# Performance work log

Measured on AMD Instinct MI355X. Metric: run time of the kernel, lower is better.

## Reference

```python
import jax, jax.numpy as jnp
import numpy as np

V, L, H, E, S = 50257, 12, 12, 768, 1024
B, T = 4, 1024
D = E // H
EPS = 1e-5


def setup_inputs() -> dict:
    key = jax.random.key(0)
    ks = jax.random.split(key, 16)
    n = lambda k, shape: (jax.random.normal(k, shape, dtype=jnp.float32) * 0.02)
    return {
        'idx': jax.random.randint(ks[0], (B, T), 0, V),
        'wte': n(ks[1], (V, E)),
        'wpe': n(ks[2], (S, E)),
        'ln1_g': jnp.ones((L, E)), 'ln1_b': jnp.zeros((L, E)),
        'attn_w': n(ks[3], (L, E, 3 * E)), 'attn_b': jnp.zeros((L, 3 * E)),
        'proj_w': n(ks[4], (L, E, E)), 'proj_b': jnp.zeros((L, E)),
        'ln2_g': jnp.ones((L, E)), 'ln2_b': jnp.zeros((L, E)),
        'fc_w': n(ks[5], (L, E, 4 * E)), 'fc_b': jnp.zeros((L, 4 * E)),
        'mproj_w': n(ks[6], (L, 4 * E, E)), 'mproj_b': jnp.zeros((L, E)),
        'lnf_g': jnp.ones((E,)), 'lnf_b': jnp.zeros((E,)),
    }


def layer_norm(x, g, b):
    m = jnp.mean(x, axis=-1, keepdims=True)
    v = jnp.var(x, axis=-1, keepdims=True)
    return (x - m) * jax.lax.rsqrt(v + EPS) * g + b


def reference(idx, wte, wpe, ln1_g, ln1_b, attn_w, attn_b, proj_w, proj_b,
              ln2_g, ln2_b, fc_w, fc_b, mproj_w, mproj_b, lnf_g, lnf_b):
    b, t = idx.shape
    x = wte[idx] + wpe[:t]  # [B,T,E]
    causal = jnp.tril(jnp.ones((t, t), dtype=bool))
    neg_inf = jnp.finfo(x.dtype).min
    for l in range(L):
        h = layer_norm(x, ln1_g[l], ln1_b[l])
        qkv = h @ attn_w[l] + attn_b[l]  # [B,T,3E]
        q, k, v = jnp.split(qkv, 3, axis=-1)
        q = q.reshape(b, t, H, D).transpose(0, 2, 1, 3)  # [B,H,T,D]
        k = k.reshape(b, t, H, D).transpose(0, 2, 1, 3)
        v = v.reshape(b, t, H, D).transpose(0, 2, 1, 3)
        att = jnp.einsum('bhqd,bhkd->bhqk', q, k) / jnp.sqrt(jnp.float32(D))
        att = jnp.where(causal, att, neg_inf)
        att = jax.nn.softmax(att, axis=-1)
        y = jnp.einsum('bhqk,bhkd->bhqd', att, v)
        y = y.transpose(0, 2, 1, 3).reshape(b, t, E)
        x = x + y @ proj_w[l] + proj_b[l]
        h2 = layer_norm(x, ln2_g[l], ln2_b[l])
        h2 = jax.nn.gelu(h2 @ fc_w[l] + fc_b[l], approximate=True)
        x = x + h2 @ mproj_w[l] + mproj_b[l]
    x = layer_norm(x, lnf_g, lnf_b)
    logits = x @ wte.T  # tied lm_head
    return logits
```

## Files before the change

kernel.cpp:

```cpp
#include <hip/hip_runtime.h>
#include <hip/hip_bf16.h>
#include <math.h>

#define VSZ 50257
#define VPAD2 50432
#define NLAYER 12
#define NH 12
#define EMB 768
#define TSEQ 1024
#define NB 4
#define MROWS (NB * TSEQ)
#define DHEAD 64
#define LN_EPS 1e-5f

typedef __attribute__((ext_vector_type(8))) short bf16x8;
typedef __attribute__((ext_vector_type(4))) float f32x4;

__device__ __forceinline__ void load_lds16(const void* g, void* l) {
    __builtin_amdgcn_global_load_lds((const __attribute__((address_space(1))) unsigned int*)g,
                                     (__attribute__((address_space(3))) unsigned int*)l,
                                     16, 0, 0);
}

__global__ void embed_kernel(const int* __restrict__ idx, const float* __restrict__ wte,
                             const float* __restrict__ wpe, float* __restrict__ x) {
    int row = blockIdx.x;
    int t = row & (TSEQ - 1);
    int tok = idx[row];
    const float* wt = wte + (size_t)tok * EMB;
    const float* wp = wpe + (size_t)t * EMB;
    float* xo = x + (size_t)row * EMB;
    for (int e = threadIdx.x; e < EMB; e += blockDim.x)
        xo[e] = wt[e] + wp[e];
}

__global__ void ln_kernel(const float* __restrict__ x, const float* __restrict__ g,
                          const float* __restrict__ b, __hip_bfloat16* __restrict__ out) {
    int row = blockIdx.x;
    const float* xr = x + (size_t)row * EMB;
    __hip_bfloat16* yr = out + (size_t)row * EMB;
    int tid = threadIdx.x;
    float v0 = xr[tid], v1 = xr[tid + 256], v2 = xr[tid + 512];
    float s = v0 + v1 + v2;
    float ss = v0 * v0 + v1 * v1 + v2 * v2;
    #pragma unroll
    for (int i = 1; i < 64; i <<= 1) {
        s  += __shfl_xor(s, i, 64);
        ss += __shfl_xor(ss, i, 64);
    }
    __shared__ float sm[4], sv[4];
    int lane = tid & 63, wid = tid >> 6;
    if (lane == 0) { sm[wid] = s; sv[wid] = ss; }
    __syncthreads();
    float sum = sm[0] + sm[1] + sm[2] + sm[3];
    float sqs = sv[0] + sv[1] + sv[2] + sv[3];
    float mean = sum * (1.0f / EMB);
    float var = sqs * (1.0f / EMB) - mean * mean;
    float rstd = rsqrtf(var + LN_EPS);
    yr[tid]       = __float2bfloat16((v0 - mean) * rstd * g[tid]       + b[tid]);
    yr[tid + 256] = __float2bfloat16((v1 - mean) * rstd * g[tid + 256] + b[tid + 256]);
    yr[tid + 512] = __float2bfloat16((v2 - mean) * rstd * g[tid + 512] + b[tid + 512]);
}

__global__ void ln_acc_kernel(float* __restrict__ x, const float* __restrict__ p0,
                              const float* __restrict__ p1,
                              const float* __restrict__ g, const float* __restrict__ b,
                              __hip_bfloat16* __restrict__ out) {
    int row = blockIdx.x;
    float* xr = x + (size_t)row * EMB;
    const float* q0 = p0 + (size_t)row * EMB;
    const float* q1 = p1 + (size_t)row * EMB;
    __hip_bfloat16* yr = out + (size_t)row * EMB;
    int tid = threadIdx.x;
    float v0 = xr[tid]       + q0[tid]       + q1[tid];
    float v1 = xr[tid + 256] + q0[tid + 256] + q1[tid + 256];
    float v2 = xr[tid + 512] + q0[tid + 512] + q1[tid + 512];
    xr[tid] = v0; xr[tid + 256] = v1; xr[tid + 512] = v2;
    float s = v0 + v1 + v2;
    float ss = v0 * v0 + v1 * v1 + v2 * v2;
    #pragma unroll
    for (int i = 1; i < 64; i <<= 1) {
        s  += __shfl_xor(s, i, 64);
        ss += __shfl_xor(ss, i, 64);
    }
    __shared__ float sm[4], sv[4];
    int lane = tid & 63, wid = tid >> 6;
    if (lane == 0) { sm[wid] = s; sv[wid] = ss; }
    __syncthreads();
    float sum = sm[0] + sm[1] + sm[2] + sm[3];
    float sqs = sv[0] + sv[1] + sv[2] + sv[3];
    float mean = sum * (1.0f / EMB);
    float var = sqs * (1.0f / EMB) - mean * mean;
    float rstd = rsqrtf(var + LN_EPS);
    yr[tid]       = __float2bfloat16((v0 - mean) * rstd * g[tid]       + b[tid]);
    yr[tid + 256] = __float2bfloat16((v1 - mean) * rstd * g[tid + 256] + b[tid + 256]);
    yr[tid + 512] = __float2bfloat16((v2 - mean) * rstd * g[tid + 512] + b[tid + 512]);
}

__global__ void convT4_kernel(const float* __restrict__ aw, const float* __restrict__ pw,
                              const float* __restrict__ fw, const float* __restrict__ mw,
                              __hip_bfloat16* __restrict__ awT, __hip_bfloat16* __restrict__ pwT,
                              __hip_bfloat16* __restrict__ fwT, __hip_bfloat16* __restrict__ mwT) {
    __shared__ float tile[32][33];
    int bid = blockIdx.x;
    const float* W; __hip_bfloat16* Wt; int K, N, t;
    if (bid < 1728)      { W = aw; Wt = awT; K = 768;  N = 2304; t = bid; }
    else if (bid < 2304) { W = pw; Wt = pwT; K = 768;  N = 768;  t = bid - 1728; }
    else if (bid < 4608) { W = fw; Wt = fwT; K = 768;  N = 3072; t = bid - 2304; }
    else                 { W = mw; Wt = mwT; K = 3072; N = 768;  t = bid - 4608; }
    int NT = N >> 5;
    int n0 = (t % NT) << 5, k0 = (t / NT) << 5;
    int tx = threadIdx.x & 31, ty = threadIdx.x >> 5;
    #pragma unroll
    for (int i = ty; i < 32; i += 8)
        tile[i][tx] = W[(size_t)(k0 + i) * N + n0 + tx];
    __syncthreads();
    #pragma unroll
    for (int i = ty; i < 32; i += 8)
        Wt[(size_t)(n0 + i) * K + k0 + tx] = __float2bfloat16(tile[tx][i]);
}

__global__ void conv_wte_kernel(const float* __restrict__ wte, __hip_bfloat16* __restrict__ o) {
    int row = blockIdx.x;
    bool pad = row >= VSZ;
    const float* src = wte + (size_t)row * EMB;
    __hip_bfloat16* dst = o + (size_t)row * EMB;
    for (int e = threadIdx.x; e < EMB; e += blockDim.x)
        dst[e] = __float2bfloat16(pad ? 0.0f : src[e]);
}

template <bool GELU, bool RES, int OUT, bool SPLITK>
__global__ __launch_bounds__(512) void gemm_bt(
                        const __hip_bfloat16* __restrict__ A, const __hip_bfloat16* __restrict__ B,
                        const float* __restrict__ bias, const float* __restrict__ res,
                        float* __restrict__ Cf, __hip_bfloat16* __restrict__ Cb,
                        __hip_bfloat16* __restrict__ vt, float* __restrict__ Cp1,
                        int Kc, int lda, int ldc, int Nclip) {
    __shared__ __hip_bfloat16 Ash[128 * 64];
    __shared__ __hip_bfloat16 Bsh[128 * 64];
    const int tid = threadIdx.x;
    const int lane = tid & 63, wid = tid >> 6;
    const int wr = wid >> 2, wc = wid & 3;

    const int nwg_all = gridDim.x;
    const int cpx = nwg_all >> 3;
    int wg = (blockIdx.x & 7) * cpx + (blockIdx.x >> 3);
    int chunk = 0, nwg = nwg_all;
    if (SPLITK) { chunk = wg & 1; wg >>= 1; nwg = nwg_all >> 1; }
    const int NT = nwg >> 5;
    const int bandsz = NT << 3;
    const int band = wg / bandsz;
    const int rem = wg - band * bandsz;
    const int m0 = (band * 8 + (rem & 7)) * 128;
    const int n0 = (rem >> 3) * 128;
    const int koff = SPLITK ? chunk * Kc : 0;

    f32x4 acc[4][2] = {};
    const int srow = lane >> 3;
    const int scol = ((lane & 7) ^ srow) * 8;

    const int lr16 = lane & 15;
    const int hi = lane >> 4;

    for (int k0 = 0; k0 < Kc; k0 += 64) {
        #pragma unroll
        for (int it = 0; it < 2; ++it) {
            int c = wid + it * 8;
            const __hip_bfloat16* ga = A + (size_t)(m0 + c * 8 + srow) * lda + koff + k0 + scol;
            load_lds16(ga, &Ash[c * 512]);
            const __hip_bfloat16* gb = B + (size_t)(n0 + c * 8 + srow) * lda + koff + k0 + scol;
            load_lds16(gb, &Bsh[c * 512]);
        }
        __syncthreads();
        bf16x8 a[4][2], b[2][2];
        #pragma unroll
        for (int m = 0; m < 4; ++m)
            #pragma unroll
            for (int kk = 0; kk < 2; ++kk) {
                int ra = wr * 64 + m * 16 + lr16;
                int ca = (kk * 32 + hi * 8) ^ ((ra & 7) * 8);
                a[m][kk] = *(const bf16x8*)&Ash[ra * 64 + ca];
            }
        #pragma unroll
        for (int n = 0; n < 2; ++n)
            #pragma unroll
            for (int kk = 0; kk < 2; ++kk) {
                int rb = wc * 32 + n * 16 + lr16;
                int cb = (kk * 32 + hi * 8) ^ ((rb & 7) * 8);
                b[n][kk] = *(const bf16x8*)&Bsh[rb * 64 + cb];
            }
        #pragma unroll
        for (int kk = 0; kk < 2; ++kk)
            #pragma unroll
            for (int m = 0; m < 4; ++m)
                #pragma unroll
                for (int n = 0; n < 2; ++n)
                    acc[m][n] = __builtin_amdgcn_mfma_f32_16x16x32_bf16(a[m][kk], b[n][kk], acc[m][n], 0, 0, 0);
        __syncthreads();
    }

    float* Co = (SPLITK && chunk) ? Cp1 : Cf;
    const bool dobias = bias && (!SPLITK || chunk == 0);
    const int crow0 = m0 + wr * 64, ccol0 = n0 + wc * 32;
    #pragma unroll
    for (int m = 0; m < 4; ++m) {
        #pragma unroll
        for (int n = 0; n < 2; ++n) {
            int col = ccol0 + n * 16 + lr16;
            if (col >= Nclip) continue;
            float bv = dobias ? bias[col] : 0.0f;
            #pragma unroll
            for (int j = 0; j < 4; ++j) {
                int r = crow0 + m * 16 + hi * 4 + j;
                float v = acc[m][n][j] + bv;
                if (GELU) {
                    float t = 0.7978845608028654f * (v + 0.044715f * v * v * v);
                    v = 0.5f * v * (1.0f + tanhf(t));
                }
                if (RES) v += res[(size_t)r * ldc + col];
                if (OUT == 0) Co[(size_t)r * ldc + col] = v;
                else if (OUT == 1) Cb[(size_t)r * ldc + col] = __float2bfloat16(v);
                else {
                    if (col < 2 * EMB) Cb[(size_t)r * (2 * EMB) + col] = __float2bfloat16(v);
                    else {
                        int hh = (col - 2 * EMB) >> 6, dd = (col - 2 * EMB) & 63;
                        int bb = r >> 10, tt = r & 1023;
                        vt[(((size_t)bb * NH + hh) * 64 + dd) * TSEQ + tt] = __float2bfloat16(v);
                    }
                }
            }
        }
    }
}

#define G256_STAGE_A(KT, MH, P) do { \
    int ktw_ = (KT) % 12; \
    load_lds16(A + (size_t)(m0 + (MH) * 64 + srow) * 768 + ktw_ * 64 + sgr8, \
               &lds[(P) * 2][(MH) * 8192 + wid * 512]); \
    load_lds16(A + (size_t)(m0 + 128 + (MH) * 64 + srow) * 768 + ktw_ * 64 + sgr8, \
               &lds[(P) * 2][(MH) * 8192 + 4096 + wid * 512]); \
} while (0)

#define G256_STAGE_B(KT, NH, P) do { \
    int ktw_ = (KT) % 12; \
    load_lds16(Bm + (size_t)(bwc0 * 64 + (NH) * 32 + brow) * 768 + ktw_ * 64 + sgr8, \
               &lds[(P) * 2 + 1][(NH) * 8192 + wid * 512]); \
    load_lds16(Bm + (size_t)((2 + bwc0) * 64 + (NH) * 32 + brow) * 768 + ktw_ * 64 + sgr8, \
               &lds[(P) * 2 + 1][(NH) * 8192 + 4096 + wid * 512]); \
} while (0)

#define G256_PHASE(MH, NH, P, STAGE_STMT, VM) do { \
    bf16x8 af[4][2], bf[2][2]; \
    _Pragma("unroll") \
    for (int f = 0; f < 4; ++f) \
        _Pragma("unroll") \
        for (int kk = 0; kk < 2; ++kk) { \
            int pr = (MH) * 128 + wr * 64 + f * 16 + lr16; \
            af[f][kk] = *(const bf16x8*)((const char*)lds[(P) * 2] + pr * 128 + ((kk * 64 + hi * 16) ^ ((lr16 & 7) << 4))); \
        } \
    _Pragma("unroll") \
    for (int nn = 0; nn < 2; ++nn) \
        _Pragma("unroll") \
        for (int kk = 0; kk < 2; ++kk) { \
            int pr = (NH) * 128 + wc * 32 + nn * 16 + lr16; \
            bf[nn][kk] = *(const bf16x8*)((const char*)lds[(P) * 2 + 1] + pr * 128 + ((kk * 64 + hi * 16) ^ ((lr16 & 7) << 4))); \
        } \
    STAGE_STMT; \
    asm volatile("s_waitcnt vmcnt(" #VM ")" ::: "memory"); \
    __builtin_amdgcn_s_barrier(); \
    asm volatile("s_waitcnt lgkmcnt(0)" ::: "memory"); \
    __builtin_amdgcn_sched_barrier(0); \
    __builtin_amdgcn_s_setprio(1); \
    _Pragma("unroll") \
    for (int kk = 0; kk < 2; ++kk) \
        _Pragma("unroll") \
        for (int f = 0; f < 4; ++f) \
            _Pragma("unroll") \
            for (int nn = 0; nn < 2; ++nn) \
                acc[(MH) * 4 + f][(NH) * 2 + nn] = __builtin_amdgcn_mfma_f32_16x16x32_bf16( \
                    af[f][kk], bf[nn][kk], acc[(MH) * 4 + f][(NH) * 2 + nn], 0, 0, 0); \
    __builtin_amdgcn_s_setprio(0); \
    __builtin_amdgcn_s_barrier(); \
} while (0)

__global__ __launch_bounds__(512, 1) void gemm256(const __hip_bfloat16* __restrict__ A,
                                                  const __hip_bfloat16* __restrict__ Bw,
                                                  float* __restrict__ C) {
    __shared__ __hip_bfloat16 lds[4][16384];
    const int tid = threadIdx.x;
    const int lane = tid & 63, wid = tid >> 6;
    const int wr = wid >> 2, wc = wid & 3;
    const int lr16 = lane & 15, hi = lane >> 4;

    const int bid = blockIdx.x;
    const int wg = (bid & 7) * 394 + (bid >> 3);
    const int band = wg / 1576, rem = wg % 1576;
    const int mt = band * 8 + (rem & 7), nt = rem >> 3;
    const size_t m0 = (size_t)mt * 256;
    const __hip_bfloat16* Bm = Bw + (size_t)nt * 256 * 768;

    const int srow = tid >> 3;
    const int sgr8 = ((tid & 7) ^ ((tid >> 3) & 7)) * 8;
    const int brow = (tid >> 3) & 31;
    const int bwc0 = tid >> 8;

    f32x4 acc[8][4] = {};

    G256_STAGE_A(0, 0, 0);
    G256_STAGE_B(0, 0, 0);
    G256_STAGE_A(0, 1, 0);
    G256_STAGE_B(0, 1, 0);
    G256_STAGE_A(1, 0, 1);
    G256_STAGE_B(1, 0, 1);
    asm volatile("s_waitcnt vmcnt(8)" ::: "memory");
    __builtin_amdgcn_s_barrier();

    for (int kt2 = 0; kt2 < 12; kt2 += 2) {
        G256_PHASE(0, 0, 0, G256_STAGE_A(kt2 + 1, 1, 1), 6);
        G256_PHASE(0, 1, 0, G256_STAGE_B(kt2 + 1, 1, 1), 10);
        G256_PHASE(1, 0, 0, G256_STAGE_A(kt2 + 2, 0, 0), 10);
        G256_PHASE(1, 1, 0, G256_STAGE_B(kt2 + 2, 0, 0), 8);
        G256_PHASE(0, 0, 1, G256_STAGE_A(kt2 + 2, 1, 0), 6);
        G256_PHASE(0, 1, 1, G256_STAGE_B(kt2 + 2, 1, 0), 10);
        G256_PHASE(1, 0, 1, G256_STAGE_A(kt2 + 3, 0, 1), 10);
        G256_PHASE(1, 1, 1, G256_STAGE_B(kt2 + 3, 0, 1), 8);
    }

    const int ccol0 = nt * 256 + wc * 64;
    #pragma unroll
    for (int mf = 0; mf < 8; ++mf) {
        size_t row = m0 + wr * 128 + (mf >> 2) * 64 + (mf & 3) * 16 + hi * 4;
        #pragma unroll
        for (int nf = 0; nf < 4; ++nf) {
            int col = ccol0 + nf * 16 + lr16;
            if (col < VSZ) {
                #pragma unroll
                for (int j = 0; j < 4; ++j)
                    C[(row + j) * VSZ + col] = acc[mf][nf][j];
            }
        }
    }
}

__global__ __launch_bounds__(256) void flash_attn(const __hip_bfloat16* __restrict__ qk,
                                                  const __hip_bfloat16* __restrict__ vT,
                                                  __hip_bfloat16* __restrict__ y) {
    const int qt = blockIdx.x, h = blockIdx.y, b = blockIdx.z;
    const int tid = threadIdx.x;
    const int lane = tid & 63, w = tid >> 6;
    const int g = lane >> 4, lr = lane & 15;

    __shared__ char KshB[64 * 128];
    __shared__ char VshB[64 * 128];
    __shared__ char PshB[4][16 * 128];

    const __hip_bfloat16* qrow = qk + ((size_t)(b * TSEQ + qt * 64 + w * 16 + lr)) * 1536 + h * 64;
    bf16x8 qf0 = *(const bf16x8*)(qrow + g * 8);
    bf16x8 qf1 = *(const bf16x8*)(qrow + 32 + g * 8);

    float m[4], l[4];
    f32x4 o[4];
    #pragma unroll
    for (int j = 0; j < 4; ++j) { m[j] = -1e30f; l[j] = 0.0f; }
    #pragma unroll
    for (int n = 0; n < 4; ++n) o[n] = (f32x4){0.f, 0.f, 0.f, 0.f};

    const int r0 = tid >> 3;
    const int c0 = (tid & 7) * 8;

    for (int kt = 0; kt <= qt; ++kt) {
        __syncthreads();
        #pragma unroll
        for (int it = 0; it < 2; ++it) {
            int r = r0 + it * 32;
            bf16x8 kv = *(const bf16x8*)(qk + ((size_t)(b * TSEQ + kt * 64 + r)) * 1536 + EMB + h * 64 + c0);
            *(bf16x8*)(KshB + ((r * 128 + c0 * 2) ^ ((r & 7) << 4))) = kv;
            bf16x8 vv = *(const bf16x8*)(vT + (((size_t)(b * NH + h)) * 64 + r) * TSEQ + kt * 64 + c0);
            *(bf16x8*)(VshB + ((r * 128 + c0 * 2) ^ ((r & 7) << 4))) = vv;
        }
        __syncthreads();

        f32x4 s[4] = {};
        #pragma unroll
        for (int n = 0; n < 4; ++n) {
            int kr = n * 16 + lr;
            bf16x8 kb0 = *(const bf16x8*)(KshB + ((kr * 128 + g * 16) ^ ((kr & 7) << 4)));
            bf16x8 kb1 = *(const bf16x8*)(KshB + ((kr * 128 + 64 + g * 16) ^ ((kr & 7) << 4)));
            s[n] = __builtin_amdgcn_mfma_f32_16x16x32_bf16(qf0, kb0, s[n], 0, 0, 0);
            s[n] = __builtin_amdgcn_mfma_f32_16x16x32_bf16(qf1, kb1, s[n], 0, 0, 0);
        }

        const bool diag = (kt == qt);
        float tmax[4] = {-1e30f, -1e30f, -1e30f, -1e30f};
        #pragma unroll
        for (int n = 0; n < 4; ++n)
            #pragma unroll
            for (int j = 0; j < 4; ++j) {
                float v = s[n][j] * 0.125f;
                if (diag && (n * 16 + lr > w * 16 + g * 4 + j)) v = -1e30f;
                s[n][j] = v;
                tmax[j] = fmaxf(tmax[j], v);
            }
        #pragma unroll
        for (int j = 0; j < 4; ++j)
            #pragma unroll
            for (int i = 1; i < 16; i <<= 1)
                tmax[j] = fmaxf(tmax[j], __shfl_xor(tmax[j], i, 64));

        float lsum[4] = {0.f, 0.f, 0.f, 0.f};
        float pexp[4][4];
        #pragma unroll
        for (int j = 0; j < 4; ++j) {
            float mn = fmaxf(m[j], tmax[j]);
            float sc = __expf(m[j] - mn);
            l[j] *= sc;
            m[j] = mn;
            #pragma unroll
            for (int n = 0; n < 4; ++n) {
                float p = __expf(s[n][j] - mn);
                pexp[n][j] = p;
                lsum[j] += p;
                o[n][j] *= sc;
            }
        }
        #pragma unroll
        for (int j = 0; j < 4; ++j) {
            #pragma unroll
            for (int i = 1; i < 16; i <<= 1) lsum[j] += __shfl_xor(lsum[j], i, 64);
            l[j] += lsum[j];
        }

        char* P = PshB[w];
        #pragma unroll
        for (int n = 0; n < 4; ++n)
            #pragma unroll
            for (int j = 0; j < 4; ++j) {
                int rw = g * 4 + j;
                *(__hip_bfloat16*)(P + ((rw * 128 + (n * 16 + lr) * 2) ^ ((rw & 7) << 4))) =
                    __float2bfloat16(pexp[n][j]);
            }
        asm volatile("s_waitcnt lgkmcnt(0)" ::: "memory");
        bf16x8 pa0 = *(const bf16x8*)(P + ((lr * 128 + g * 16) ^ ((lr & 7) << 4)));
        bf16x8 pa1 = *(const bf16x8*)(P + ((lr * 128 + 64 + g * 16) ^ ((lr & 7) << 4)));
        #pragma unroll
        for (int n = 0; n < 4; ++n) {
            int vr = n * 16 + lr;
            bf16x8 vb0 = *(const bf16x8*)(VshB + ((vr * 128 + g * 16) ^ ((vr & 7) << 4)));
            bf16x8 vb1 = *(const bf16x8*)(VshB + ((vr * 128 + 64 + g * 16) ^ ((vr & 7) << 4)));
            o[n] = __builtin_amdgcn_mfma_f32_16x16x32_bf16(pa0, vb0, o[n], 0, 0, 0);
            o[n] = __builtin_amdgcn_mfma_f32_16x16x32_bf16(pa1, vb1, o[n], 0, 0, 0);
        }
    }

    #pragma unroll
    for (int j = 0; j < 4; ++j) {
        float inv = 1.0f / l[j];
        int row = b * TSEQ + qt * 64 + w * 16 + g * 4 + j;
        #pragma unroll
        for (int n = 0; n < 4; ++n)
            y[(size_t)row * EMB + h * 64 + n * 16 + lr] = __float2bfloat16(o[n][j] * inv);
    }
}

extern "C" void kernel_launch(void* const* d_in, const int* in_sizes, int n_in,
                              void* d_out, int out_size, void* d_ws, size_t ws_size,
                              hipStream_t stream) {
    const int*   idx     = (const int*)d_in[0];
    const float* wte     = (const float*)d_in[1];
    const float* wpe     = (const float*)d_in[2];
    const float* ln1_g   = (const float*)d_in[3];
    const float* ln1_b   = (const float*)d_in[4];
    const float* attn_w  = (const float*)d_in[5];
    const float* attn_b  = (const float*)d_in[6];
    const float* proj_w  = (const float*)d_in[7];
    const float* proj_b  = (const float*)d_in[8];
    const float* ln2_g   = (const float*)d_in[9];
    const float* ln2_b   = (const float*)d_in[10];
    const float* fc_w    = (const float*)d_in[11];
    const float* fc_b    = (const float*)d_in[12];
    const float* mproj_w = (const float*)d_in[13];
    const float* mproj_b = (const float*)d_in[14];
    const float* lnf_g   = (const float*)d_in[15];
    const float* lnf_b   = (const float*)d_in[16];
    float* out = (float*)d_out;

    char* w = (char*)d_ws;
    float* x = (float*)w;                      w += (size_t)MROWS * EMB * 4;
    float* p0 = (float*)w;                     w += (size_t)MROWS * EMB * 4;
    float* p1 = (float*)w;                     w += (size_t)MROWS * EMB * 4;
    __hip_bfloat16* qkb = (__hip_bfloat16*)w;  w += (size_t)MROWS * 2 * EMB * 2;
    __hip_bfloat16* vTb = (__hip_bfloat16*)w;  w += (size_t)NB * NH * 64 * TSEQ * 2;
    __hip_bfloat16* h = (__hip_bfloat16*)w;    w += (size_t)MROWS * EMB * 2;
    __hip_bfloat16* y = (__hip_bfloat16*)w;    w += (size_t)MROWS * EMB * 2;
    __hip_bfloat16* g = (__hip_bfloat16*)w;    w += (size_t)MROWS * 4 * EMB * 2;
    __hip_bfloat16* wqkvT = (__hip_bfloat16*)w;   w += (size_t)3 * EMB * EMB * 2;
    __hip_bfloat16* wprojT = (__hip_bfloat16*)w;  w += (size_t)EMB * EMB * 2;
    __hip_bfloat16* wfcT = (__hip_bfloat16*)w;    w += (size_t)4 * EMB * EMB * 2;
    __hip_bfloat16* wmprojT = (__hip_bfloat16*)w; w += (size_t)4 * EMB * EMB * 2;
    __hip_bfloat16* wteB = (__hip_bfloat16*)w;    w += (size_t)VPAD2 * EMB * 2;

    dim3 blk256(256), blk512(512);

    embed_kernel<<<MROWS, blk256, 0, stream>>>(idx, wte, wpe, x);
    conv_wte_kernel<<<VPAD2, blk256, 0, stream>>>(wte, wteB);

    for (int l = 0; l < NLAYER; l++) {
        const float* aw = attn_w + (size_t)l * EMB * 3 * EMB;
        const float* ab = attn_b + (size_t)l * 3 * EMB;
        const float* pw = proj_w + (size_t)l * EMB * EMB;
        const float* pb = proj_b + (size_t)l * EMB;
        const float* fw = fc_w   + (size_t)l * EMB * 4 * EMB;
        const float* fb = fc_b   + (size_t)l * 4 * EMB;
        const float* mw = mproj_w + (size_t)l * 4 * EMB * EMB;
        const float* mb = mproj_b + (size_t)l * EMB;

        if (l == 0)
            ln_kernel<<<MROWS, blk256, 0, stream>>>(x, ln1_g + l * EMB, ln1_b + l * EMB, h);
        else
            ln_acc_kernel<<<MROWS, blk256, 0, stream>>>(x, p0, p1, ln1_g + l * EMB, ln1_b + l * EMB, h);

        convT4_kernel<<<6912, blk256, 0, stream>>>(aw, pw, fw, mw, wqkvT, wprojT, wfcT, wmprojT);

        gemm_bt<false, false, 2, false><<<dim3((3 * EMB / 128) * 32), blk512, 0, stream>>>(
            h, wqkvT, ab, nullptr, nullptr, qkb, vTb, nullptr, EMB, EMB, 3 * EMB, 3 * EMB);

        flash_attn<<<dim3(TSEQ / 64, NH, NB), blk256, 0, stream>>>(qkb, vTb, y);

        gemm_bt<false, false, 0, true><<<dim3((EMB / 128) * 32 * 2), blk512, 0, stream>>>(
            y, wprojT, pb, nullptr, p0, nullptr, nullptr, p1, EMB / 2, EMB, EMB, EMB);

        ln_acc_kernel<<<MROWS, blk256, 0, stream>>>(x, p0, p1, ln2_g + l * EMB, ln2_b + l * EMB, h);

        gemm_bt<true, false, 1, false><<<dim3((4 * EMB / 128) * 32), blk512, 0, stream>>>(
            h, wfcT, fb, nullptr, nullptr, g, nullptr, nullptr, EMB, EMB, 4 * EMB, 4 * EMB);

        gemm_bt<false, false, 0, true><<<dim3((EMB / 128) * 32 * 2), blk512, 0, stream>>>(
            g, wmprojT, mb, nullptr, p0, nullptr, nullptr, p1, 2 * EMB, 4 * EMB, EMB, EMB);
    }

    ln_acc_kernel<<<MROWS, blk256, 0, stream>>>(x, p0, p1, lnf_g, lnf_b, h);

    gemm256<<<dim3((VPAD2 / 256) * (MROWS / 256)), dim3(512), 0, stream>>>(h, wteB, out);
}
```

Before: 2.828 ms.

## Replace 256-tile LM-head GEMM with generic 128-tile GEMM using nontemporal stores

Removes the dedicated 256x256 ping-pong pipelined gemm256 kernel for the tied LM head. It reuses the generic 128x128 gemm_bt kernel with a band width of 16 row tiles and a new output mode that writes the large fp32 logits with nontemporal stores. The aim is to keep the huge logits write from polluting the cache and to improve L2 reuse of the wte tiles through the wider band. The cost is giving up the larger tile's arithmetic intensity and its hand-tuned software pipeline.

```diff
diff --git a/kernel.cpp b/kernel.cpp
--- a/kernel.cpp
+++ b/kernel.cpp
@@ -129,7 +129,7 @@
         dst[e] = __float2bfloat16(pad ? 0.0f : src[e]);
 }
 
-template <bool GELU, bool RES, int OUT, bool SPLITK>
+template <bool GELU, bool RES, int OUT, bool SPLITK, int BAND = 8>
 __global__ __launch_bounds__(512) void gemm_bt(
                         const __hip_bfloat16* __restrict__ A, const __hip_bfloat16* __restrict__ B,
                         const float* __restrict__ bias, const float* __restrict__ res,
@@ -148,11 +148,11 @@
     int chunk = 0, nwg = nwg_all;
     if (SPLITK) { chunk = wg & 1; wg >>= 1; nwg = nwg_all >> 1; }
     const int NT = nwg >> 5;
-    const int bandsz = NT << 3;
+    const int bandsz = NT * BAND;
     const int band = wg / bandsz;
     const int rem = wg - band * bandsz;
-    const int m0 = (band * 8 + (rem & 7)) * 128;
-    const int n0 = (rem >> 3) * 128;
+    const int m0 = (band * BAND + (rem & (BAND - 1))) * 128;
+    const int n0 = (rem / BAND) * 128;
     const int koff = SPLITK ? chunk * Kc : 0;
 
     f32x4 acc[4][2] = {};
@@ -219,6 +219,7 @@
                 }
                 if (RES) v += res[(size_t)r * ldc + col];
                 if (OUT == 0) Co[(size_t)r * ldc + col] = v;
+                else if (OUT == 3) __builtin_nontemporal_store(v, &Co[(size_t)r * ldc + col]);
                 else if (OUT == 1) Cb[(size_t)r * ldc + col] = __float2bfloat16(v);
                 else {
                     if (col < 2 * EMB) Cb[(size_t)r * (2 * EMB) + col] = __float2bfloat16(v);
@@ -228,115 +229,6 @@
                         vt[(((size_t)bb * NH + hh) * 64 + dd) * TSEQ + tt] = __float2bfloat16(v);
                     }
                 }
-            }
-        }
-    }
-}
-
-#define G256_STAGE_A(KT, MH, P) do { \
-    int ktw_ = (KT) % 12; \
-    load_lds16(A + (size_t)(m0 + (MH) * 64 + srow) * 768 + ktw_ * 64 + sgr8, \
-               &lds[(P) * 2][(MH) * 8192 + wid * 512]); \
-    load_lds16(A + (size_t)(m0 + 128 + (MH) * 64 + srow) * 768 + ktw_ * 64 + sgr8, \
-               &lds[(P) * 2][(MH) * 8192 + 4096 + wid * 512]); \
-} while (0)
-
-#define G256_STAGE_B(KT, NH, P) do { \
-    int ktw_ = (KT) % 12; \
-    load_lds16(Bm + (size_t)(bwc0 * 64 + (NH) * 32 + brow) * 768 + ktw_ * 64 + sgr8, \
-               &lds[(P) * 2 + 1][(NH) * 8192 + wid * 512]); \
-    load_lds16(Bm + (size_t)((2 + bwc0) * 64 + (NH) * 32 + brow) * 768 + ktw_ * 64 + sgr8, \
-               &lds[(P) * 2 + 1][(NH) * 8192 + 4096 + wid * 512]); \
-} while (0)
-
-#define G256_PHASE(MH, NH, P, STAGE_STMT, VM) do { \
-    bf16x8 af[4][2], bf[2][2]; \
-    _Pragma("unroll") \
-    for (int f = 0; f < 4; ++f) \
-        _Pragma("unroll") \
-        for (int kk = 0; kk < 2; ++kk) { \
-            int pr = (MH) * 128 + wr * 64 + f * 16 + lr16; \
-            af[f][kk] = *(const bf16x8*)((const char*)lds[(P) * 2] + pr * 128 + ((kk * 64 + hi * 16) ^ ((lr16 & 7) << 4))); \
-        } \
-    _Pragma("unroll") \
-    for (int nn = 0; nn < 2; ++nn) \
-        _Pragma("unroll") \
-        for (int kk = 0; kk < 2; ++kk) { \
-            int pr = (NH) * 128 + wc * 32 + nn * 16 + lr16; \
-            bf[nn][kk] = *(const bf16x8*)((const char*)lds[(P) * 2 + 1] + pr * 128 + ((kk * 64 + hi * 16) ^ ((lr16 & 7) << 4))); \
-        } \
-    STAGE_STMT; \
-    asm volatile("s_waitcnt vmcnt(" #VM ")" ::: "memory"); \
-    __builtin_amdgcn_s_barrier(); \
-    asm volatile("s_waitcnt lgkmcnt(0)" ::: "memory"); \
-    __builtin_amdgcn_sched_barrier(0); \
-    __builtin_amdgcn_s_setprio(1); \
-    _Pragma("unroll") \
-    for (int kk = 0; kk < 2; ++kk) \
-        _Pragma("unroll") \
-        for (int f = 0; f < 4; ++f) \
-            _Pragma("unroll") \
-            for (int nn = 0; nn < 2; ++nn) \
-                acc[(MH) * 4 + f][(NH) * 2 + nn] = __builtin_amdgcn_mfma_f32_16x16x32_bf16( \
-                    af[f][kk], bf[nn][kk], acc[(MH) * 4 + f][(NH) * 2 + nn], 0, 0, 0); \
-    __builtin_amdgcn_s_setprio(0); \
-    __builtin_amdgcn_s_barrier(); \
-} while (0)
-
-__global__ __launch_bounds__(512, 1) void gemm256(const __hip_bfloat16* __restrict__ A,
-                                                  const __hip_bfloat16* __restrict__ Bw,
-                                                  float* __restrict__ C) {
-    __shared__ __hip_bfloat16 lds[4][16384];
-    const int tid = threadIdx.x;
-    const int lane = tid & 63, wid = tid >> 6;
-    const int wr = wid >> 2, wc = wid & 3;
-    const int lr16 = lane & 15, hi = lane >> 4;
-
-    const int bid = blockIdx.x;
-    const int wg = (bid & 7) * 394 + (bid >> 3);
-    const int band = wg / 1576, rem = wg % 1576;
-    const int mt = band * 8 + (rem & 7), nt = rem >> 3;
-    const size_t m0 = (size_t)mt * 256;
-    const __hip_bfloat16* Bm = Bw + (size_t)nt * 256 * 768;
-
-    const int srow = tid >> 3;
-    const int sgr8 = ((tid & 7) ^ ((tid >> 3) & 7)) * 8;
-    const int brow = (tid >> 3) & 31;
-    const int bwc0 = tid >> 8;
-
-    f32x4 acc[8][4] = {};
-
-    G256_STAGE_A(0, 0, 0);
-    G256_STAGE_B(0, 0, 0);
-    G256_STAGE_A(0, 1, 0);
-    G256_STAGE_B(0, 1, 0);
-    G256_STAGE_A(1, 0, 1);
-    G256_STAGE_B(1, 0, 1);
-    asm volatile("s_waitcnt vmcnt(8)" ::: "memory");
-    __builtin_amdgcn_s_barrier();
-
-    for (int kt2 = 0; kt2 < 12; kt2 += 2) {
-        G256_PHASE(0, 0, 0, G256_STAGE_A(kt2 + 1, 1, 1), 6);
-        G256_PHASE(0, 1, 0, G256_STAGE_B(kt2 + 1, 1, 1), 10);
-        G256_PHASE(1, 0, 0, G256_STAGE_A(kt2 + 2, 0, 0), 10);
-        G256_PHASE(1, 1, 0, G256_STAGE_B(kt2 + 2, 0, 0), 8);
-        G256_PHASE(0, 0, 1, G256_STAGE_A(kt2 + 2, 1, 0), 6);
-        G256_PHASE(0, 1, 1, G256_STAGE_B(kt2 + 2, 1, 0), 10);
-        G256_PHASE(1, 0, 1, G256_STAGE_A(kt2 + 3, 0, 1), 10);
-        G256_PHASE(1, 1, 1, G256_STAGE_B(kt2 + 3, 0, 1), 8);
-    }
-
-    const int ccol0 = nt * 256 + wc * 64;
-    #pragma unroll
-    for (int mf = 0; mf < 8; ++mf) {
-        size_t row = m0 + wr * 128 + (mf >> 2) * 64 + (mf & 3) * 16 + hi * 4;
-        #pragma unroll
-        for (int nf = 0; nf < 4; ++nf) {
-            int col = ccol0 + nf * 16 + lr16;
-            if (col < VSZ) {
-                #pragma unroll
-                for (int j = 0; j < 4; ++j)
-                    C[(row + j) * VSZ + col] = acc[mf][nf][j];
             }
         }
     }
@@ -540,5 +432,6 @@
 
     ln_acc_kernel<<<MROWS, blk256, 0, stream>>>(x, p0, p1, lnf_g, lnf_b, h);
 
-    gemm256<<<dim3((VPAD2 / 256) * (MROWS / 256)), dim3(512), 0, stream>>>(h, wteB, out);
-}
+    gemm_bt<false, false, 3, false, 16><<<dim3((VPAD2 / 128) * 32), blk512, 0, stream>>>(
+        h, wteB, nullptr, nullptr, out, nullptr, nullptr, nullptr, EMB, EMB, VSZ, VSZ);
+}
```

After: 3.173 ms. 12.2% more time.
